# Kernel tuning notes

Measured on AMD Instinct MI355X. Metric: run time of the kernel, lower is better.

Reference implementation:

```python
import jax, jax.numpy as jnp
import numpy as np

BS = 16
CTX_PER = 1024   # local context nodes per proof state
ARGS_PER = 32    # arguments per proof state
KEY_DIM = 128
D_MODEL = 512


def setup_inputs() -> dict:
    key = jax.random.key(0)
    k1, k2, k3 = jax.random.split(key, 3)
    n_ctx = BS * CTX_PER
    n_args = BS * ARGS_PER
    # segment ids: sorted, uniform segments (static ragged structure)
    ctx_ids = jnp.repeat(jnp.arange(BS, dtype=jnp.int32), CTX_PER)
    arg_ids = jnp.repeat(jnp.arange(BS, dtype=jnp.int32), ARGS_PER)
    arg_values = jax.random.normal(k1, (n_args, KEY_DIM), dtype=jnp.float32)
    ctx_values = jax.random.normal(k2, (n_ctx, D_MODEL), dtype=jnp.float32)
    W = jax.random.normal(k3, (D_MODEL, KEY_DIM), dtype=jnp.float32) / np.sqrt(D_MODEL)
    b = jnp.zeros((KEY_DIM,), dtype=jnp.float32)
    return {"bs": BS, "arg_ids": arg_ids, "ctx_ids": ctx_ids,
            "arg_values": arg_values, "ctx_values": ctx_values, "W": W, "b": b}


def reference(bs, arg_ids, ctx_ids, arg_values, ctx_values, W, b):
    n_args = arg_ids.shape[0]
    n_ctx = ctx_ids.shape[0]
    # total (arg, ctx-element) pairs; static because segments are uniform by construction
    P = n_args * (n_ctx // bs)

    # ctx_lens[s] = number of context elements in proof state s
    ctx_lens = jax.ops.segment_sum(jnp.ones_like(ctx_ids), ctx_ids, num_segments=bs)
    arg_ctx_lens = ctx_lens[arg_ids]                      # [n_args]

    # ragged-range construction: row id + within-row offset for each flat pair
    arg_ends = jnp.cumsum(arg_ctx_lens)                   # inclusive cumsum
    arg_starts = arg_ends - arg_ctx_lens                  # exclusive cumsum
    pos = jnp.arange(P, dtype=arg_ends.dtype)
    rows = jnp.searchsorted(arg_ends, pos, side='right')  # value_rowids  [P]
    offs = pos - arg_starts[rows]                         # ragged range values [P]

    # column index into flat context values
    ctx_starts = jnp.cumsum(ctx_lens) - ctx_lens          # exclusive cumsum [bs]
    cols = ctx_starts[arg_ids[rows]] + offs               # [P]

    keys_all = ctx_values @ W + b                         # Dense key projection [n_ctx, key_dim]
    queries = arg_values[rows]                            # [P, key_dim]
    keys = keys_all[cols]                                 # [P, key_dim]
    logits_flat = jnp.einsum('pd,pd->p', queries, keys)   # [P]
    return rows.astype(jnp.int32), logits_flat
```

## Files before the change

kernel.cpp:

```cpp
#include <hip/hip_runtime.h>


#define BSZ        16
#define CTX_PER    1024
#define ARGS_PER   32
#define KD         128
#define DM         512
#define N_ARGS     (BSZ * ARGS_PER)
#define P_TOTAL    (N_ARGS * CTX_PER)

typedef __attribute__((ext_vector_type(8))) short short8;
typedef __attribute__((ext_vector_type(4))) float float4v;

__device__ inline short bf16_of(float x) {
    unsigned u = __builtin_bit_cast(unsigned, x);
    unsigned r = (u + 0x7fffu + ((u >> 16) & 1u)) >> 16;
    return (short)r;
}

__device__ inline short8 cvt8(float4 lo, float4 hi) {
    short8 r;
    r[0] = bf16_of(lo.x); r[1] = bf16_of(lo.y); r[2] = bf16_of(lo.z); r[3] = bf16_of(lo.w);
    r[4] = bf16_of(hi.x); r[5] = bf16_of(hi.y); r[6] = bf16_of(hi.z); r[7] = bf16_of(hi.w);
    return r;
}

__global__ __launch_bounds__(256) void qproj_kernel(
    const float* __restrict__ arg, const float* __restrict__ W,
    const float* __restrict__ b, short* __restrict__ Qp, float* __restrict__ qb)
{
    const int t = threadIdx.x, lane = t & 63, wave = t >> 6;
    const int mtile = blockIdx.x >> 3;
    const int ntile = (blockIdx.x & 7) * 4 + wave;
    const int n = lane & 15, quad = lane >> 4;

    const float* asrc = arg + (size_t)(mtile * 16 + n) * KD + quad * 8;
    short8 afr[4];
    #pragma unroll
    for (int kt = 0; kt < 4; ++kt)
        afr[kt] = cvt8(*(const float4*)(asrc + kt * 32), *(const float4*)(asrc + kt * 32 + 4));

    const float* wsrc = W + (size_t)(ntile * 16 + n) * KD + quad * 8;
    float4v acc = {0.f, 0.f, 0.f, 0.f};
    #pragma unroll
    for (int kt = 0; kt < 4; ++kt) {
        short8 bfr = cvt8(*(const float4*)(wsrc + kt * 32), *(const float4*)(wsrc + kt * 32 + 4));
        acc = __builtin_amdgcn_mfma_f32_16x16x32_bf16(afr[kt], bfr, acc, 0, 0, 0);
    }
    #pragma unroll
    for (int r = 0; r < 4; ++r)
        Qp[(size_t)(mtile * 16 + quad * 4 + r) * DM + ntile * 16 + n] = bf16_of(acc[r]);

    if ((blockIdx.x & 7) == 0) {
        __shared__ float red[16][17];
        const int al = t >> 4, seg = t & 15;
        const float* qrow = arg + (size_t)(mtile * 16 + al) * KD + seg * 8;
        float p = 0.f;
        #pragma unroll
        for (int j = 0; j < 8; ++j) p += qrow[j] * b[seg * 8 + j];
        red[al][seg] = p;
        __syncthreads();
        if (t < 16) {
            float ssum = 0.f;
            #pragma unroll
            for (int j = 0; j < 16; ++j) ssum += red[t][j];
            qb[mtile * 16 + t] = ssum;
        }
    }
}

__global__ __launch_bounds__(256, 4) void main_kernel(
    const float* __restrict__ ctx, const short* __restrict__ Qp,
    const float* __restrict__ qb, float* __restrict__ out)
{
    __shared__ __align__(16) short Qpl[32][520];

    const int t = threadIdx.x, lane = t & 63, wave = t >> 6;
    const int s = blockIdx.x >> 6;
    const int chunk = blockIdx.x & 63;

    {
        const short* src = Qp + (size_t)s * 32 * DM;
        #pragma unroll
        for (int i = 0; i < 8; ++i) {
            const int u = i * 256 + t;
            const int row = u >> 6, c = u & 63;
            *(float4*)&Qpl[row][c * 8] = *(const float4*)(src + (size_t)row * DM + c * 8);
        }
    }
    __syncthreads();

    const int n = lane & 15, quad = lane >> 4;
    const int k0 = wave * 128;
    const float* crow = ctx + (size_t)(s * CTX_PER + chunk * 16 + n) * DM + k0 + quad * 8;

    float4v acc0 = {0.f, 0.f, 0.f, 0.f};
    float4v acc1 = {0.f, 0.f, 0.f, 0.f};
    #pragma unroll
    for (int kt = 0; kt < 4; ++kt) {
        float4 c0 = *(const float4*)(crow + kt * 32);
        float4 c1 = *(const float4*)(crow + kt * 32 + 4);
        short8 bfr = cvt8(c0, c1);
        short8 a0 = *(const short8*)&Qpl[n][k0 + kt * 32 + quad * 8];
        short8 a1 = *(const short8*)&Qpl[16 + n][k0 + kt * 32 + quad * 8];
        acc0 = __builtin_amdgcn_mfma_f32_16x16x32_bf16(a0, bfr, acc0, 0, 0, 0);
        acc1 = __builtin_amdgcn_mfma_f32_16x16x32_bf16(a1, bfr, acc1, 0, 0, 0);
    }

    __syncthreads();
    float* Sp = (float*)&Qpl[0][0];
    #pragma unroll
    for (int r = 0; r < 4; ++r) {
        Sp[wave * 512 + (quad * 4 + r) * 16 + n]      = acc0[r];
        Sp[wave * 512 + (16 + quad * 4 + r) * 16 + n] = acc1[r];
    }
    __syncthreads();

    const int a = t >> 3, c2 = (t & 7) * 2;
    const int base = a * 16 + c2;
    float v0 = Sp[base]        + Sp[512 + base]     + Sp[1024 + base]     + Sp[1536 + base];
    float v1 = Sp[base + 1]    + Sp[512 + base + 1] + Sp[1024 + base + 1] + Sp[1536 + base + 1];
    const int ga = s * ARGS_PER + a;
    const float qbv = qb[ga];
    const size_t off = (size_t)ga * CTX_PER + chunk * 16 + c2;
    *(float2*)(out + P_TOTAL + off) = make_float2(v0 + qbv, v1 + qbv);
    *(float2*)(out + off)           = make_float2((float)ga, (float)ga);
}

extern "C" void kernel_launch(void* const* d_in, const int* in_sizes, int n_in,
                              void* d_out, int out_size, void* d_ws, size_t ws_size,
                              hipStream_t stream)
{
    const float* arg_values = (const float*)d_in[3];
    const float* ctx_values = (const float*)d_in[4];
    const float* W          = (const float*)d_in[5];
    const float* b          = (const float*)d_in[6];
    float* out = (float*)d_out;

    short* Qp = (short*)d_ws;
    float* qb = (float*)((char*)d_ws + (size_t)N_ARGS * DM * sizeof(short));

    qproj_kernel<<<256, 256, 0, stream>>>(arg_values, W, b, Qp, qb);
    main_kernel<<<BSZ * 64, 256, 0, stream>>>(ctx_values, Qp, qb, out);
}
```

Measured before the change: 94.18 us.

## Process two ctx chunks per block with LDS staging and prefetch overlap

```diff
diff --git a/kernel.cpp b/kernel.cpp
--- a/kernel.cpp
+++ b/kernel.cpp
@@ -69,62 +69,88 @@
     }
 }
 
-__global__ __launch_bounds__(256, 4) void main_kernel(
+__global__ __launch_bounds__(256, 2) void main_kernel(
     const float* __restrict__ ctx, const short* __restrict__ Qp,
     const float* __restrict__ qb, float* __restrict__ out)
 {
-    __shared__ __align__(16) short Qpl[32][520];
+    __shared__ __align__(16) short Cxl[2][16][520];
+    __shared__ float Sp[4][544];
 
     const int t = threadIdx.x, lane = t & 63, wave = t >> 6;
-    const int s = blockIdx.x >> 6;
-    const int chunk = blockIdx.x & 63;
+    const int s = blockIdx.x >> 5;
+    const int grp = blockIdx.x & 31;
+    const int n = lane & 15, quad = lane >> 4;
+    const int k0 = wave * 128;
 
+    short8 afr[2][4];
     {
-        const short* src = Qp + (size_t)s * 32 * DM;
+        const short* qsrc = Qp + (size_t)(s * 32 + n) * DM + k0 + quad * 8;
         #pragma unroll
-        for (int i = 0; i < 8; ++i) {
-            const int u = i * 256 + t;
-            const int row = u >> 6, c = u & 63;
-            *(float4*)&Qpl[row][c * 8] = *(const float4*)(src + (size_t)row * DM + c * 8);
-        }
+        for (int mt = 0; mt < 2; ++mt)
+            #pragma unroll
+            for (int kt = 0; kt < 4; ++kt)
+                afr[mt][kt] = *(const short8*)(qsrc + (size_t)mt * 16 * DM + kt * 32);
     }
+
+    const float* cbase = ctx + (size_t)(s * CTX_PER + grp * 32) * DM;
+    const int srow = t >> 6, sc8 = t & 63;
+    #pragma unroll
+    for (int i = 0; i < 4; ++i) {
+        const float* p = cbase + (size_t)(i * 4 + srow) * DM + sc8 * 8;
+        *(short8*)&Cxl[0][i * 4 + srow][sc8 * 8] = cvt8(*(const float4*)p, *(const float4*)(p + 4));
+    }
+
+    const int a_red = t >> 3;
+    const int c2 = (t & 7) * 2;
+    const int ga = s * ARGS_PER + a_red;
+    const float qbv = qb[ga];
+    const float2 rowsv = make_float2((float)ga, (float)ga);
+
     __syncthreads();
 
-    const int n = lane & 15, quad = lane >> 4;
-    const int k0 = wave * 128;
-    const float* crow = ctx + (size_t)(s * CTX_PER + chunk * 16 + n) * DM + k0 + quad * 8;
+    #pragma unroll
+    for (int c = 0; c < 2; ++c) {
+        float4 pf[8];
+        if (c == 0) {
+            #pragma unroll
+            for (int i = 0; i < 4; ++i) {
+                const float* p = cbase + (size_t)(16 + i * 4 + srow) * DM + sc8 * 8;
+                pf[2 * i]     = *(const float4*)p;
+                pf[2 * i + 1] = *(const float4*)(p + 4);
+            }
+        }
 
-    float4v acc0 = {0.f, 0.f, 0.f, 0.f};
-    float4v acc1 = {0.f, 0.f, 0.f, 0.f};
-    #pragma unroll
-    for (int kt = 0; kt < 4; ++kt) {
-        float4 c0 = *(const float4*)(crow + kt * 32);
-        float4 c1 = *(const float4*)(crow + kt * 32 + 4);
-        short8 bfr = cvt8(c0, c1);
-        short8 a0 = *(const short8*)&Qpl[n][k0 + kt * 32 + quad * 8];
-        short8 a1 = *(const short8*)&Qpl[16 + n][k0 + kt * 32 + quad * 8];
-        acc0 = __builtin_amdgcn_mfma_f32_16x16x32_bf16(a0, bfr, acc0, 0, 0, 0);
-        acc1 = __builtin_amdgcn_mfma_f32_16x16x32_bf16(a1, bfr, acc1, 0, 0, 0);
+        float4v acc0 = {0.f, 0.f, 0.f, 0.f};
+        float4v acc1 = {0.f, 0.f, 0.f, 0.f};
+        #pragma unroll
+        for (int kt = 0; kt < 4; ++kt) {
+            short8 bfr = *(const short8*)&Cxl[c][n][k0 + kt * 32 + quad * 8];
+            acc0 = __builtin_amdgcn_mfma_f32_16x16x32_bf16(afr[0][kt], bfr, acc0, 0, 0, 0);
+            acc1 = __builtin_amdgcn_mfma_f32_16x16x32_bf16(afr[1][kt], bfr, acc1, 0, 0, 0);
+        }
+
+        if (c == 0) {
+            #pragma unroll
+            for (int i = 0; i < 4; ++i)
+                *(short8*)&Cxl[1][i * 4 + srow][sc8 * 8] = cvt8(pf[2 * i], pf[2 * i + 1]);
+        }
+
+        #pragma unroll
+        for (int r = 0; r < 4; ++r) {
+            Sp[wave][(quad * 4 + r) * 17 + n]        = acc0[r];
+            Sp[wave][(16 + quad * 4 + r) * 17 + n]   = acc1[r];
+        }
+        __syncthreads();
+
+        const int base = a_red * 17 + c2;
+        float v0 = Sp[0][base]     + Sp[1][base]     + Sp[2][base]     + Sp[3][base];
+        float v1 = Sp[0][base + 1] + Sp[1][base + 1] + Sp[2][base + 1] + Sp[3][base + 1];
+        const size_t off = (size_t)ga * CTX_PER + grp * 32 + c * 16 + c2;
+        *(float2*)(out + P_TOTAL + off) = make_float2(v0 + qbv, v1 + qbv);
+        *(float2*)(out + off)           = rowsv;
+
+        if (c == 0) __syncthreads();
     }
-
-    __syncthreads();
-    float* Sp = (float*)&Qpl[0][0];
-    #pragma unroll
-    for (int r = 0; r < 4; ++r) {
-        Sp[wave * 512 + (quad * 4 + r) * 16 + n]      = acc0[r];
-        Sp[wave * 512 + (16 + quad * 4 + r) * 16 + n] = acc1[r];
-    }
-    __syncthreads();
-
-    const int a = t >> 3, c2 = (t & 7) * 2;
-    const int base = a * 16 + c2;
-    float v0 = Sp[base]        + Sp[512 + base]     + Sp[1024 + base]     + Sp[1536 + base];
-    float v1 = Sp[base + 1]    + Sp[512 + base + 1] + Sp[1024 + base + 1] + Sp[1536 + base + 1];
-    const int ga = s * ARGS_PER + a;
-    const float qbv = qb[ga];
-    const size_t off = (size_t)ga * CTX_PER + chunk * 16 + c2;
-    *(float2*)(out + P_TOTAL + off) = make_float2(v0 + qbv, v1 + qbv);
-    *(float2*)(out + off)           = make_float2((float)ga, (float)ga);
 }
 
 extern "C" void kernel_launch(void* const* d_in, const int* in_sizes, int n_in,
@@ -141,5 +167,5 @@
     float* qb = (float*)((char*)d_ws + (size_t)N_ARGS * DM * sizeof(short));
 
     qproj_kernel<<<256, 256, 0, stream>>>(arg_values, W, b, Qp, qb);
-    main_kernel<<<BSZ * 64, 256, 0, stream>>>(ctx_values, Qp, qb, out);
+    main_kernel<<<BSZ * 32, 256, 0, stream>>>(ctx_values, Qp, qb, out);
 }
```

New measurement: 93.06 us. No clear change (-1.2%).
